# Optimization experiments

Measured on AMD Instinct MI355X. Metric: run time of the kernel, lower is better.

## Reference

```python
import jax, jax.numpy as jnp
import numpy as np

N_NODES = 50000


def _gcn_conv(x, W, b, src, dst, n):
    # PyG GCNConv: h = x @ W, symmetric-normalized aggregation, then + bias.
    h = x @ W  # [N, out]
    deg = jax.ops.segment_sum(jnp.ones_like(dst, dtype=h.dtype), dst, num_segments=n)
    dinv = jnp.where(deg > 0, jax.lax.rsqrt(jnp.maximum(deg, 1e-12)), 0.0)
    norm = dinv[src] * dinv[dst]  # [E]
    msg = h[src] * norm[:, None]  # gather + scale, [E, out]
    out = jax.ops.segment_sum(msg, dst, num_segments=n)
    return out + b


def setup_inputs() -> dict:
    key = jax.random.key(0)
    ks = jax.random.split(key, 8)
    d_in, d_h, d_out = 256, 256, 128
    E = 800000
    x = jax.random.normal(ks[0], (N_NODES, d_in), dtype=jnp.float32)
    edge_index = jax.random.randint(ks[1], (2, E), 0, N_NODES, dtype=jnp.int64)
    def glorot(k, shape):
        lim = np.sqrt(6.0 / (shape[0] + shape[1]))
        return jax.random.uniform(k, shape, jnp.float32, -lim, lim)
    return {
        "x": x,
        "edge_index": edge_index,
        "W1": glorot(ks[2], (d_in, d_h)), "b1": jnp.zeros((d_h,), jnp.float32),
        "W2": glorot(ks[3], (d_h, d_h)), "b2": jnp.zeros((d_h,), jnp.float32),
        "W3": glorot(ks[4], (d_h, d_out)), "b3": jnp.zeros((d_out,), jnp.float32),
    }


def reference(x, edge_index, W1, b1, W2, b2, W3, b3):
    n = x.shape[0]
    # add self-loops once (PyG GCNConv default add_self_loops=True)
    loop = jnp.arange(n, dtype=edge_index.dtype)
    src = jnp.concatenate([edge_index[0], loop])
    dst = jnp.concatenate([edge_index[1], loop])
    h = _gcn_conv(x, W1, b1, src, dst, n)
    h = jax.nn.relu(h)  # dropout is identity in eval mode
    h = _gcn_conv(h, W2, b2, src, dst, n)
    h = jax.nn.relu(h)
    h = _gcn_conv(h, W3, b3, src, dst, n)
    return h
```

## Files before the change

### kernel.cpp

```cpp
#include <hip/hip_runtime.h>
#include <stdint.h>

typedef short v8s __attribute__((ext_vector_type(8)));
typedef float v4f __attribute__((ext_vector_type(4)));
typedef float v2f __attribute__((ext_vector_type(2)));

#define MAXDEG 64
#define CSTRIDE 16

__device__ inline unsigned short f2bf(float f) {
    union { float f; unsigned u; } c; c.f = f;
    unsigned u = c.u;
    unsigned r = (u + 0x7FFFu + ((u >> 16) & 1u)) >> 16;
    return (unsigned short)r;
}
__device__ inline void gl_lds16(const unsigned short* g, unsigned short* l) {
    __builtin_amdgcn_global_load_lds(
        (const __attribute__((address_space(1))) unsigned int*)(g),
        (__attribute__((address_space(3))) unsigned int*)(l), 16, 0, 0);
}

__global__ void k_pre1(const int* __restrict__ src, const int* __restrict__ dst, int E,
                       int* __restrict__ cnt, int* __restrict__ col,
                       const float* __restrict__ x, unsigned short* __restrict__ A,
                       int n, int mpad,
                       const float* __restrict__ W1, const float* __restrict__ W2,
                       const float* __restrict__ W3, unsigned short* __restrict__ Wt,
                       int gE, int gX) {
    int b = blockIdx.x;
    if (b < gE) {
        int e = b * 256 + threadIdx.x;
        if (e < E) {
            int d = dst[e];
            int p = atomicAdd(&cnt[(size_t)d * CSTRIDE], 1);
            if (p < MAXDEG) col[(size_t)d * MAXDEG + p] = src[e];
        }
    } else if (b < gE + gX) {
        int g = (b - gE) * 256 + threadIdx.x;
        int total = mpad * 64;
        if (g >= total) return;
        int row = g >> 6;
        float4 v;
        if (row < n) v = ((const float4*)x)[(size_t)g];
        else v = make_float4(0.f, 0.f, 0.f, 0.f);
        ushort4 o;
        o.x = f2bf(v.x); o.y = f2bf(v.y); o.z = f2bf(v.z); o.w = f2bf(v.w);
        ((ushort4*)A)[(size_t)g] = o;
    } else {
        int idx = (b - gE - gX) * 256 + threadIdx.x;
        const float* W; int base, N;
        if (idx < 65536)       { W = W1; base = 0;      N = 256; }
        else if (idx < 131072) { W = W2; base = 65536;  N = 256; }
        else                   { W = W3; base = 131072; N = 128; }
        int loc = idx - base;
        int nn = loc >> 8;
        int k = loc & 255;
        Wt[idx] = f2bf(W[(size_t)k * N + nn]);
    }
}

__launch_bounds__(256, 4)
__global__ void k_gemm(const unsigned short* __restrict__ A,
                       const unsigned short* __restrict__ Wt,
                       unsigned short* __restrict__ Hs,
                       const int* __restrict__ cnt, int n, int N) {
    __shared__ unsigned short sA[128 * 32];
    __shared__ unsigned short sB[128 * 32];
    const int t = threadIdx.x;
    const int lane = t & 63;
    const int wave = t >> 6;
    const int wm = wave >> 1, wn = wave & 1;
    const int m0 = blockIdx.x * 128;
    const int n0 = blockIdx.y * 128;

    v4f acc[4][4];
#pragma unroll
    for (int i = 0; i < 4; i++)
#pragma unroll
        for (int j = 0; j < 4; j++)
#pragma unroll
            for (int r = 0; r < 4; r++) acc[i][j][r] = 0.f;

    const int c0 = t, c1 = t + 256;
    const int r0 = c0 >> 2, kc0 = (c0 & 3) * 8;
    const int r1 = c1 >> 2, kc1 = (c1 & 3) * 8;
    const size_t aBase0 = (size_t)(m0 + r0) * 256 + kc0;
    const size_t aBase1 = (size_t)(m0 + r1) * 256 + kc1;
    const size_t bBase0 = (size_t)(n0 + r0) * 256 + kc0;
    const size_t bBase1 = (size_t)(n0 + r1) * 256 + kc1;

    const int q = lane >> 4;
    const int lm = lane & 15;

    for (int k0 = 0; k0 < 256; k0 += 32) {
        __syncthreads();
        gl_lds16(A + aBase0 + k0, &sA[c0 * 8]);
        gl_lds16(A + aBase1 + k0, &sA[c1 * 8]);
        gl_lds16(Wt + bBase0 + k0, &sB[c0 * 8]);
        gl_lds16(Wt + bBase1 + k0, &sB[c1 * 8]);
        __syncthreads();

        v8s afr[4], bfr[4];
#pragma unroll
        for (int i = 0; i < 4; i++) {
            int r = wm * 64 + i * 16 + lm;
            afr[i] = *(const v8s*)&sA[r * 32 + q * 8];
        }
#pragma unroll
        for (int j = 0; j < 4; j++) {
            int nn = wn * 64 + j * 16 + lm;
            bfr[j] = *(const v8s*)&sB[nn * 32 + q * 8];
        }
#pragma unroll
        for (int i = 0; i < 4; i++)
#pragma unroll
            for (int j = 0; j < 4; j++)
                acc[i][j] = __builtin_amdgcn_mfma_f32_16x16x32_bf16(afr[i], bfr[j],
                                                                    acc[i][j], 0, 0, 0);
    }

#pragma unroll
    for (int i = 0; i < 4; i++) {
        int mbase = m0 + wm * 64 + i * 16 + q * 4;
#pragma unroll
        for (int r = 0; r < 4; r++) {
            int m = mbase + r;
            float s = (m < n) ? rsqrtf((float)(cnt[(size_t)m * CSTRIDE] + 1)) : 0.f;
#pragma unroll
            for (int j = 0; j < 4; j++) {
                int colI = n0 + wn * 64 + j * 16 + lm;
                Hs[(size_t)m * N + colI] = f2bf(acc[i][j][r] * s);
            }
        }
    }
}

template <int D, int CS, bool RELU, bool F32OUT>
__launch_bounds__(256, 8)
__global__ void k_agg(const unsigned short* __restrict__ Hs,
                      const int* __restrict__ cnt, const int* __restrict__ col,
                      const float* __restrict__ bias,
                      unsigned short* __restrict__ outb, float* __restrict__ outf,
                      int n, int nzero) {
    constexpr int LPN = CS / 8;
    constexpr int NPG = 64 / LPN;
    const int lane = threadIdx.x & 63;
    const int i = blockIdx.x * 4 + (threadIdx.x >> 6);
    const int ch0 = blockIdx.y * CS;
    if (i >= n) return;
    const int g = lane / LPN;
    const int cl = lane % LPN;

    v2f acc[4];
#pragma unroll
    for (int k = 0; k < 4; k++) acc[k] = (v2f){0.f, 0.f};

    auto accq = [&](unsigned u, int k) {
        union { unsigned uu; float f; } lo, hi;
        lo.uu = u << 16;
        hi.uu = u & 0xffff0000u;
        v2f t; t[0] = lo.f; t[1] = hi.f;
        acc[k] += t;
    };
    auto acc16 = [&](uint4 q) { accq(q.x, 0); accq(q.y, 1); accq(q.z, 2); accq(q.w, 3); };

    const unsigned short* base = Hs + ch0 + cl * 8;
    const int deg = cnt[(size_t)i * CSTRIDE];
    const size_t cbase = (size_t)i * MAXDEG;
    const int T = deg + 1;
    const int Tpad = (T + NPG - 1) & ~(NPG - 1);

    for (int b = 0; b < Tpad; b += 64) {
        int t = b + lane;
        int v;
        if (t == 0) v = i;
        else if (t <= deg) v = col[cbase + t - 1];
        else v = nzero;
        int lim = min(64, Tpad - b);
        int t2 = 0;
        for (; t2 + 4 * NPG <= lim; t2 += 4 * NPG) {
            int c0 = __shfl(v, t2 + 0 * NPG + g);
            int c1 = __shfl(v, t2 + 1 * NPG + g);
            int c2 = __shfl(v, t2 + 2 * NPG + g);
            int c3 = __shfl(v, t2 + 3 * NPG + g);
            uint4 q0 = *(const uint4*)(base + (size_t)c0 * D);
            uint4 q1 = *(const uint4*)(base + (size_t)c1 * D);
            uint4 q2 = *(const uint4*)(base + (size_t)c2 * D);
            uint4 q3 = *(const uint4*)(base + (size_t)c3 * D);
            acc16(q0); acc16(q1); acc16(q2); acc16(q3);
        }
        for (; t2 + 2 * NPG <= lim; t2 += 2 * NPG) {
            int c0 = __shfl(v, t2 + 0 * NPG + g);
            int c1 = __shfl(v, t2 + 1 * NPG + g);
            uint4 q0 = *(const uint4*)(base + (size_t)c0 * D);
            uint4 q1 = *(const uint4*)(base + (size_t)c1 * D);
            acc16(q0); acc16(q1);
        }
        for (; t2 + NPG <= lim; t2 += NPG) {
            int c0 = __shfl(v, t2 + g);
            uint4 q0 = *(const uint4*)(base + (size_t)c0 * D);
            acc16(q0);
        }
    }

#pragma unroll
    for (int off = LPN; off < 64; off <<= 1) {
#pragma unroll
        for (int k = 0; k < 4; k++) {
            acc[k][0] += __shfl_xor(acc[k][0], off);
            acc[k][1] += __shfl_xor(acc[k][1], off);
        }
    }

    if (g == 0) {
        float di = rsqrtf((float)(deg + 1));
        float o[8];
#pragma unroll
        for (int k = 0; k < 4; k++) {
            o[2 * k + 0] = di * acc[k][0] + bias[ch0 + cl * 8 + 2 * k + 0];
            o[2 * k + 1] = di * acc[k][1] + bias[ch0 + cl * 8 + 2 * k + 1];
        }
        if (RELU) {
#pragma unroll
            for (int k = 0; k < 8; k++) o[k] = fmaxf(o[k], 0.f);
        }
        if constexpr (F32OUT) {
            float* p = outf + (size_t)i * D + ch0 + cl * 8;
            *(float4*)p = make_float4(o[0], o[1], o[2], o[3]);
            *(float4*)(p + 4) = make_float4(o[4], o[5], o[6], o[7]);
        } else {
            uint4 q;
            q.x = ((unsigned)f2bf(o[1]) << 16) | f2bf(o[0]);
            q.y = ((unsigned)f2bf(o[3]) << 16) | f2bf(o[2]);
            q.z = ((unsigned)f2bf(o[5]) << 16) | f2bf(o[4]);
            q.w = ((unsigned)f2bf(o[7]) << 16) | f2bf(o[6]);
            *(uint4*)(outb + (size_t)i * D + ch0 + cl * 8) = q;
        }
    }
}

extern "C" void kernel_launch(void* const* d_in, const int* in_sizes, int n_in,
                              void* d_out, int out_size, void* d_ws, size_t ws_size,
                              hipStream_t stream) {
    const float* x  = (const float*)d_in[0];
    const int*   ei = (const int*)d_in[1];
    const float* W1 = (const float*)d_in[2];
    const float* b1 = (const float*)d_in[3];
    const float* W2 = (const float*)d_in[4];
    const float* b2 = (const float*)d_in[5];
    const float* W3 = (const float*)d_in[6];
    const float* b3 = (const float*)d_in[7];

    const int n = in_sizes[0] / 256;
    const int E = in_sizes[1] / 2;
    const int mpad = ((n + 127) / 128) * 128;

    char* ws = (char*)d_ws;
    size_t off = 0;
    auto alloc = [&](size_t bytes) -> void* {
        void* p = ws + off;
        off += (bytes + 255) & ~(size_t)255;
        return p;
    };
    int* cnt      = (int*)alloc((size_t)mpad * CSTRIDE * 4);
    int* col      = (int*)alloc((size_t)n * MAXDEG * 4);
    unsigned short* Wt = (unsigned short*)alloc((size_t)163840 * 2);
    unsigned short* W1t = Wt;
    unsigned short* W2t = Wt + 65536;
    unsigned short* W3t = Wt + 131072;
    unsigned short* bufA = (unsigned short*)alloc((size_t)mpad * 256 * 2);
    unsigned short* bufB = (unsigned short*)alloc((size_t)mpad * 256 * 2);
    (void)ws_size; (void)n_in; (void)out_size;

    const int* srcp = ei;
    const int* dstp = ei + E;
    const int gE = (E + 255) / 256;
    const int gX = (mpad * 64 + 255) / 256;
    const int gW = 640;

    hipMemsetAsync(cnt, 0, (size_t)n * CSTRIDE * 4, stream);

    k_pre1<<<gE + gX + gW, 256, 0, stream>>>(srcp, dstp, E, cnt, col, x, bufA, n, mpad,
                                             W1, W2, W3, Wt, gE, gX);

    const int gAgg = (n + 3) / 4;
    dim3 gg1(mpad / 128, 2);
    k_gemm<<<gg1, 256, 0, stream>>>(bufA, W1t, bufB, cnt, n, 256);
    k_agg<256, 128, true, false><<<dim3(gAgg, 2), 256, 0, stream>>>(
        bufB, cnt, col, b1, bufA, nullptr, n, n);
    k_gemm<<<gg1, 256, 0, stream>>>(bufA, W2t, bufB, cnt, n, 256);
    k_agg<256, 128, true, false><<<dim3(gAgg, 2), 256, 0, stream>>>(
        bufB, cnt, col, b2, bufA, nullptr, n, n);
    dim3 gg3(mpad / 128, 1);
    k_gemm<<<gg3, 256, 0, stream>>>(bufA, W3t, bufB, cnt, n, 128);
    k_agg<128, 128, false, true><<<dim3(gAgg, 1), 256, 0, stream>>>(
        bufB, cnt, col, b3, nullptr, (float*)d_out, n, n);
}
```

Measured before the change: 341.7 us.

## Overlap edge bucketing with first GEMM and move layer-1 normalization into aggregation

```diff
diff --git a/kernel.cpp b/kernel.cpp
--- a/kernel.cpp
+++ b/kernel.cpp
@@ -19,35 +19,25 @@
         (const __attribute__((address_space(1))) unsigned int*)(g),
         (__attribute__((address_space(3))) unsigned int*)(l), 16, 0, 0);
 }
-
-__global__ void k_pre1(const int* __restrict__ src, const int* __restrict__ dst, int E,
-                       int* __restrict__ cnt, int* __restrict__ col,
-                       const float* __restrict__ x, unsigned short* __restrict__ A,
-                       int n, int mpad,
+__device__ inline v8s cvt8(float4 a, float4 b) {
+    v8s r;
+    r[0] = (short)f2bf(a.x); r[1] = (short)f2bf(a.y);
+    r[2] = (short)f2bf(a.z); r[3] = (short)f2bf(a.w);
+    r[4] = (short)f2bf(b.x); r[5] = (short)f2bf(b.y);
+    r[6] = (short)f2bf(b.z); r[7] = (short)f2bf(b.w);
+    return r;
+}
+
+__global__ void k_pre0(int* __restrict__ cnt, int zTotal,
                        const float* __restrict__ W1, const float* __restrict__ W2,
                        const float* __restrict__ W3, unsigned short* __restrict__ Wt,
-                       int gE, int gX) {
+                       int gZ) {
     int b = blockIdx.x;
-    if (b < gE) {
-        int e = b * 256 + threadIdx.x;
-        if (e < E) {
-            int d = dst[e];
-            int p = atomicAdd(&cnt[(size_t)d * CSTRIDE], 1);
-            if (p < MAXDEG) col[(size_t)d * MAXDEG + p] = src[e];
-        }
-    } else if (b < gE + gX) {
-        int g = (b - gE) * 256 + threadIdx.x;
-        int total = mpad * 64;
-        if (g >= total) return;
-        int row = g >> 6;
-        float4 v;
-        if (row < n) v = ((const float4*)x)[(size_t)g];
-        else v = make_float4(0.f, 0.f, 0.f, 0.f);
-        ushort4 o;
-        o.x = f2bf(v.x); o.y = f2bf(v.y); o.z = f2bf(v.z); o.w = f2bf(v.w);
-        ((ushort4*)A)[(size_t)g] = o;
+    if (b < gZ) {
+        int idx = b * 256 + threadIdx.x;
+        if (idx < zTotal) ((int4*)cnt)[idx] = make_int4(0, 0, 0, 0);
     } else {
-        int idx = (b - gE - gX) * 256 + threadIdx.x;
+        int idx = (b - gZ) * 256 + threadIdx.x;
         const float* W; int base, N;
         if (idx < 65536)       { W = W1; base = 0;      N = 256; }
         else if (idx < 131072) { W = W2; base = 65536;  N = 256; }
@@ -59,19 +49,21 @@
     }
 }
 
-__launch_bounds__(256, 4)
-__global__ void k_gemm(const unsigned short* __restrict__ A,
-                       const unsigned short* __restrict__ Wt,
-                       unsigned short* __restrict__ Hs,
-                       const int* __restrict__ cnt, int n, int N) {
+template <bool CONVA, bool SCALE>
+__device__ inline void gemm_body(int bm, int bn,
+                                 const float* __restrict__ Af,
+                                 const unsigned short* __restrict__ Ab,
+                                 const unsigned short* __restrict__ Wt,
+                                 unsigned short* __restrict__ Hs,
+                                 const int* __restrict__ cnt, int n, int N) {
     __shared__ unsigned short sA[128 * 32];
     __shared__ unsigned short sB[128 * 32];
     const int t = threadIdx.x;
     const int lane = t & 63;
     const int wave = t >> 6;
     const int wm = wave >> 1, wn = wave & 1;
-    const int m0 = blockIdx.x * 128;
-    const int n0 = blockIdx.y * 128;
+    const int m0 = bm * 128;
+    const int n0 = bn * 128;
 
     v4f acc[4][4];
 #pragma unroll
@@ -94,8 +86,22 @@
 
     for (int k0 = 0; k0 < 256; k0 += 32) {
         __syncthreads();
-        gl_lds16(A + aBase0 + k0, &sA[c0 * 8]);
-        gl_lds16(A + aBase1 + k0, &sA[c1 * 8]);
+        if constexpr (CONVA) {
+            float4 u0, u1, u2, u3;
+            if (m0 + r0 < n) {
+                u0 = *(const float4*)&Af[aBase0 + k0];
+                u1 = *(const float4*)&Af[aBase0 + k0 + 4];
+            } else { u0 = make_float4(0,0,0,0); u1 = u0; }
+            if (m0 + r1 < n) {
+                u2 = *(const float4*)&Af[aBase1 + k0];
+                u3 = *(const float4*)&Af[aBase1 + k0 + 4];
+            } else { u2 = make_float4(0,0,0,0); u3 = u2; }
+            *(v8s*)&sA[c0 * 8] = cvt8(u0, u1);
+            *(v8s*)&sA[c1 * 8] = cvt8(u2, u3);
+        } else {
+            gl_lds16(Ab + aBase0 + k0, &sA[c0 * 8]);
+            gl_lds16(Ab + aBase1 + k0, &sA[c1 * 8]);
+        }
         gl_lds16(Wt + bBase0 + k0, &sB[c0 * 8]);
         gl_lds16(Wt + bBase1 + k0, &sB[c1 * 8]);
         __syncthreads();
@@ -125,7 +131,11 @@
 #pragma unroll
         for (int r = 0; r < 4; r++) {
             int m = mbase + r;
-            float s = (m < n) ? rsqrtf((float)(cnt[(size_t)m * CSTRIDE] + 1)) : 0.f;
+            float s;
+            if constexpr (SCALE)
+                s = (m < n) ? rsqrtf((float)(cnt[(size_t)m * CSTRIDE] + 1)) : 0.f;
+            else
+                s = (m < n) ? 1.f : 0.f;
 #pragma unroll
             for (int j = 0; j < 4; j++) {
                 int colI = n0 + wn * 64 + j * 16 + lm;
@@ -135,10 +145,45 @@
     }
 }
 
-template <int D, int CS, bool RELU, bool F32OUT>
+__launch_bounds__(256, 4)
+__global__ void k_fused(const int* __restrict__ src, const int* __restrict__ dst, int E,
+                        int* __restrict__ cnt, int* __restrict__ col,
+                        const float* __restrict__ x, const unsigned short* __restrict__ W1t,
+                        unsigned short* __restrict__ Hs, int n, int gEdge) {
+    int b = blockIdx.x;
+    if (b < gEdge) {
+        int e = b * 256 + threadIdx.x;
+        if (e < E) {
+            int d = dst[e];
+            int p = atomicAdd(&cnt[(size_t)d * CSTRIDE], 1);
+            if (p < MAXDEG) col[(size_t)d * MAXDEG + p] = src[e];
+        }
+    } else {
+        int bx = b - gEdge;
+        gemm_body<true, false>(bx >> 1, bx & 1, x, nullptr, W1t, Hs, nullptr, n, 256);
+    }
+}
+
+template <bool SCALE>
+__launch_bounds__(256, 4)
+__global__ void k_gemm(const unsigned short* __restrict__ A,
+                       const unsigned short* __restrict__ Wt,
+                       unsigned short* __restrict__ Hs,
+                       const int* __restrict__ cnt, int n, int N) {
+    gemm_body<false, SCALE>(blockIdx.x, blockIdx.y, nullptr, A, Wt, Hs, cnt, n, N);
+}
+
+__global__ void k_dinv(const int* __restrict__ cnt, float* __restrict__ dinv,
+                       int n, int mpad) {
+    int i = blockIdx.x * 256 + threadIdx.x;
+    if (i < mpad) dinv[i] = (i < n) ? rsqrtf((float)(cnt[(size_t)i * CSTRIDE] + 1)) : 0.f;
+}
+
+template <int D, int CS, bool RELU, bool F32OUT, bool NSCALE>
 __launch_bounds__(256, 8)
 __global__ void k_agg(const unsigned short* __restrict__ Hs,
                       const int* __restrict__ cnt, const int* __restrict__ col,
+                      const float* __restrict__ dinv,
                       const float* __restrict__ bias,
                       unsigned short* __restrict__ outb, float* __restrict__ outf,
                       int n, int nzero) {
@@ -155,14 +200,21 @@
 #pragma unroll
     for (int k = 0; k < 4; k++) acc[k] = (v2f){0.f, 0.f};
 
-    auto accq = [&](unsigned u, int k) {
+    auto accq = [&](unsigned u, int k, float s) {
         union { unsigned uu; float f; } lo, hi;
         lo.uu = u << 16;
         hi.uu = u & 0xffff0000u;
-        v2f t; t[0] = lo.f; t[1] = hi.f;
-        acc[k] += t;
+        if constexpr (NSCALE) {
+            acc[k][0] += lo.f * s;
+            acc[k][1] += hi.f * s;
+        } else {
+            v2f t; t[0] = lo.f; t[1] = hi.f;
+            acc[k] += t;
+        }
     };
-    auto acc16 = [&](uint4 q) { accq(q.x, 0); accq(q.y, 1); accq(q.z, 2); accq(q.w, 3); };
+    auto acc16 = [&](uint4 q, float s) {
+        accq(q.x, 0, s); accq(q.y, 1, s); accq(q.z, 2, s); accq(q.w, 3, s);
+    };
 
     const unsigned short* base = Hs + ch0 + cl * 8;
     const int deg = cnt[(size_t)i * CSTRIDE];
@@ -183,23 +235,22 @@
             int c1 = __shfl(v, t2 + 1 * NPG + g);
             int c2 = __shfl(v, t2 + 2 * NPG + g);
             int c3 = __shfl(v, t2 + 3 * NPG + g);
+            float s0 = 0.f, s1 = 0.f, s2 = 0.f, s3 = 0.f;
+            if constexpr (NSCALE) {
+                s0 = dinv[c0]; s1 = dinv[c1]; s2 = dinv[c2]; s3 = dinv[c3];
+            }
             uint4 q0 = *(const uint4*)(base + (size_t)c0 * D);
             uint4 q1 = *(const uint4*)(base + (size_t)c1 * D);
             uint4 q2 = *(const uint4*)(base + (size_t)c2 * D);
             uint4 q3 = *(const uint4*)(base + (size_t)c3 * D);
-            acc16(q0); acc16(q1); acc16(q2); acc16(q3);
-        }
-        for (; t2 + 2 * NPG <= lim; t2 += 2 * NPG) {
-            int c0 = __shfl(v, t2 + 0 * NPG + g);
-            int c1 = __shfl(v, t2 + 1 * NPG + g);
-            uint4 q0 = *(const uint4*)(base + (size_t)c0 * D);
-            uint4 q1 = *(const uint4*)(base + (size_t)c1 * D);
-            acc16(q0); acc16(q1);
+            acc16(q0, s0); acc16(q1, s1); acc16(q2, s2); acc16(q3, s3);
         }
         for (; t2 + NPG <= lim; t2 += NPG) {
             int c0 = __shfl(v, t2 + g);
+            float s0 = 0.f;
+            if constexpr (NSCALE) s0 = dinv[c0];
             uint4 q0 = *(const uint4*)(base + (size_t)c0 * D);
-            acc16(q0);
+            acc16(q0, s0);
         }
     }
 
@@ -264,6 +315,7 @@
     };
     int* cnt      = (int*)alloc((size_t)mpad * CSTRIDE * 4);
     int* col      = (int*)alloc((size_t)n * MAXDEG * 4);
+    float* dinv   = (float*)alloc((size_t)mpad * 4);
     unsigned short* Wt = (unsigned short*)alloc((size_t)163840 * 2);
     unsigned short* W1t = Wt;
     unsigned short* W2t = Wt + 65536;
@@ -274,25 +326,30 @@
 
     const int* srcp = ei;
     const int* dstp = ei + E;
-    const int gE = (E + 255) / 256;
-    const int gX = (mpad * 64 + 255) / 256;
+    const int zTotal = n * CSTRIDE / 4;
+    const int gZ = (zTotal + 255) / 256;
     const int gW = 640;
-
-    hipMemsetAsync(cnt, 0, (size_t)n * CSTRIDE * 4, stream);
-
-    k_pre1<<<gE + gX + gW, 256, 0, stream>>>(srcp, dstp, E, cnt, col, x, bufA, n, mpad,
-                                             W1, W2, W3, Wt, gE, gX);
+    const int gEdge = (E + 255) / 256;
+    const int gGemm = (mpad / 128) * 2;
+
+    k_pre0<<<gZ + gW, 256, 0, stream>>>(cnt, zTotal, W1, W2, W3, Wt, gZ);
+
+    k_fused<<<gEdge + gGemm, 256, 0, stream>>>(srcp, dstp, E, cnt, col, x, W1t,
+                                               bufB, n, gEdge);
+
+    k_dinv<<<(mpad + 255) / 256, 256, 0, stream>>>(cnt, dinv, n, mpad);
 
     const int gAgg = (n + 3) / 4;
-    dim3 gg1(mpad / 128, 2);
-    k_gemm<<<gg1, 256, 0, stream>>>(bufA, W1t, bufB, cnt, n, 256);
-    k_agg<256, 128, true, false><<<dim3(gAgg, 2), 256, 0, stream>>>(
-        bufB, cnt, col, b1, bufA, nullptr, n, n);
-    k_gemm<<<gg1, 256, 0, stream>>>(bufA, W2t, bufB, cnt, n, 256);
-    k_agg<256, 128, true, false><<<dim3(gAgg, 2), 256, 0, stream>>>(
-        bufB, cnt, col, b2, bufA, nullptr, n, n);
+    k_agg<256, 128, true, false, true><<<dim3(gAgg, 2), 256, 0, stream>>>(
+        bufB, cnt, col, dinv, b1, bufA, nullptr, n, n);
+
+    dim3 gg2(mpad / 128, 2);
+    k_gemm<true><<<gg2, 256, 0, stream>>>(bufA, W2t, bufB, cnt, n, 256);
+    k_agg<256, 128, true, false, false><<<dim3(gAgg, 2), 256, 0, stream>>>(
+        bufB, cnt, col, nullptr, b2, bufA, nullptr, n, n);
+
     dim3 gg3(mpad / 128, 1);
-    k_gemm<<<gg3, 256, 0, stream>>>(bufA, W3t, bufB, cnt, n, 128);
-    k_agg<128, 128, false, true><<<dim3(gAgg, 1), 256, 0, stream>>>(
-        bufB, cnt, col, b3, nullptr, (float*)d_out, n, n);
-}
+    k_gemm<true><<<gg3, 256, 0, stream>>>(bufA, W3t, bufB, cnt, n, 128);
+    k_agg<128, 128, false, true, false><<<dim3(gAgg, 1), 256, 0, stream>>>(
+        bufB, cnt, col, nullptr, b3, nullptr, (float*)d_out, n, n);
+}
```

After: 423.1 us. +23.8%, slower.
